# Performance work log

Hardware: AMD Instinct MI355X
Metric: run time of the kernel (lower is better)

## Reference

```python
import jax, jax.numpy as jnp
import numpy as np

EDGE_TYPES = 7
TIME_STEP = 5
STATE_DIM = 1024


def setup_inputs() -> dict:
    key = jax.random.key(0)
    ks = jax.random.split(key, 8)
    B, T, N, DF = 4, 15, 15, 25600
    S, E = STATE_DIM, EDGE_TYPES
    # weights ~ N(0, 0.01), biases zero, matching _initialization()
    return {
        "pose_features": jax.random.normal(ks[0], (B, T, N, DF), jnp.float32),
        "W_compress": jax.random.normal(ks[1], (DF, S), jnp.float32) * 0.01,
        "b_compress": jnp.zeros((S,), jnp.float32),
        "W_edge": jax.random.normal(ks[2], (E, S, S), jnp.float32) * 0.01,
        "b_edge": jnp.zeros((E, S), jnp.float32),
        "W_att": jax.random.normal(ks[3], (E, 2 * S), jnp.float32) * 0.01,
        "b_att": jnp.zeros((E,), jnp.float32),
        "W_r": jax.random.normal(ks[4], (2 * S, S), jnp.float32) * 0.01,
        "b_r": jnp.zeros((S,), jnp.float32),
        "W_z": jax.random.normal(ks[5], (2 * S, S), jnp.float32) * 0.01,
        "b_z": jnp.zeros((S,), jnp.float32),
        "W_h": jax.random.normal(ks[6], (2 * S, S), jnp.float32) * 0.01,
        "b_h": jnp.zeros((S,), jnp.float32),
    }


def reference(pose_features, W_compress, b_compress, W_edge, b_edge,
              W_att, b_att, W_r, b_r, W_z, b_z, W_h, b_h):
    B, T, N, DF = pose_features.shape
    S = W_compress.shape[1]
    E = W_edge.shape[0]
    x = pose_features.reshape(B * T, N, DF)
    prop = x @ W_compress + b_compress                      # [M, N, S]
    # attention Linear over concat(row, col) == row-part + col-part (rank-1 broadcast,
    # avoids materializing the [M, N, N, 2S] repeat/cat tensor; identical math)
    Wa_row, Wa_col = W_att[:, :S], W_att[:, S:]
    scores = None
    for _ in range(1 + TIME_STEP):
        msg = jnp.einsum('bnd,edh->benh', prop, W_edge) + b_edge[None, :, None, :]  # [M,E,N,S]
        row = jnp.einsum('bend,ed->ben', msg, Wa_row)       # [M, E, N]
        col = jnp.einsum('bend,ed->ben', msg, Wa_col)
        scores = jax.nn.sigmoid(row[..., :, None] + col[..., None, :]
                                + b_att[None, :, None, None])   # [M, E, N, N]
        merged = jnp.einsum('beij,bejd->bid', scores, msg)  # [M, N, S]
        a = jnp.concatenate([merged, prop], axis=-1)        # [M, N, 2S]
        r = jax.nn.sigmoid(a @ W_r + b_r)
        z = jax.nn.sigmoid(a @ W_z + b_z)
        h_hat = jnp.tanh(jnp.concatenate([merged, r * prop], axis=-1) @ W_h + b_h)
        prop = (1 - z) * prop + z * h_hat
    box_states = scores.transpose(0, 2, 3, 1)               # [M, N, N, E]
    action_score = ((1 - box_states[..., 0:1]) * box_states).sum(axis=2)
    action_score = action_score.reshape(B, T, N, E)
    actor_score = (1 - box_states[..., 0]).reshape(B, T, N, N)
    acty_score = jax.nn.softmax(
        (action_score * actor_score.sum(axis=-1)[..., None]).sum(axis=2)[:, :, 1:],
        axis=-1)
    return action_score, acty_score, actor_score
```

## Files before the change

kernel.cpp:

```cpp
#include <hip/hip_runtime.h>
#include <hip/hip_bf16.h>

typedef unsigned short bf16_t;
typedef __bf16 bf16x8 __attribute__((ext_vector_type(8)));
typedef float f32x4 __attribute__((ext_vector_type(4)));

__device__ __forceinline__ unsigned short f2bf(float x){
  union { __hip_bfloat16 h; unsigned short u; } c;
  c.h = __float2bfloat16(x);
  return c.u;
}
__device__ __forceinline__ float bf2f(bf16_t u){
  union { unsigned short u; __hip_bfloat16 h; } c;
  c.u = u;
  return __bfloat162float(c.h);
}

#define GL2L(g, l) __builtin_amdgcn_global_load_lds( \
    (const __attribute__((address_space(1))) unsigned int*)(g), \
    (__attribute__((address_space(3))) unsigned int*)(l), 16, 0, 0)

template<int ACT, int MAP>
__global__ __launch_bounds__(256)
void gemm_bf16(const bf16_t* __restrict__ A, int lda,
               const bf16_t* __restrict__ Bt, int ldb,
               float* __restrict__ C, int ldc, size_t csplit,
               const float* __restrict__ bias,
               int M, int N, int K, int Kchunk)
{
  __shared__ __align__(16) bf16_t As[4][128*32];
  __shared__ __align__(16) bf16_t Bs[4][128*32];
  const int tid = threadIdx.x;
  const int w = tid >> 6, lane = tid & 63;
  const int wm = w >> 1, wn = w & 1;
  const int lr = lane & 15, kq = lane >> 4;
  int bcol, brow, bks;
  if (MAP == 0) { bcol = blockIdx.x; brow = blockIdx.y; bks = blockIdx.z; }
  else          { bks = blockIdx.x;  bcol = blockIdx.y; brow = blockIdx.z; }
  const int gm0 = brow * 128, gn0 = bcol * 128;
  const int k0 = bks * Kchunk;
  const int nt = (min(k0 + Kchunk, K) - k0) >> 5;

  const int srow = lane >> 2;
  const int scol = ((lane & 3) ^ ((srow >> 1) & 3)) << 3;
  const int am0 = min(gm0 + w*32 + srow,      M-1);
  const int am1 = min(gm0 + w*32 + 16 + srow, M-1);
  const int bn0 = min(gn0 + w*32 + srow,      N-1);
  const int bn1 = min(gn0 + w*32 + 16 + srow, N-1);
  const bf16_t* Ag0 = A  + (size_t)am0*lda + scol;
  const bf16_t* Ag1 = A  + (size_t)am1*lda + scol;
  const bf16_t* Bg0 = Bt + (size_t)bn0*ldb + scol;
  const bf16_t* Bg1 = Bt + (size_t)bn1*ldb + scol;

  auto STAGEF = [&](int t) {
    const int bsel = t & 3;
    const int kk = k0 + (t << 5);
    char* al = (char*)(&As[bsel][0]) + w*2048;
    char* bl = (char*)(&Bs[bsel][0]) + w*2048;
    GL2L(Ag0 + kk, al);
    GL2L(Ag1 + kk, al + 1024);
    GL2L(Bg0 + kk, bl);
    GL2L(Bg1 + kk, bl + 1024);
  };

  STAGEF(0);
  if (nt > 1) STAGEF(1);
  if (nt > 2) STAGEF(2);

  const int kqs = kq ^ ((lr >> 1) & 3);
  f32x4 acc[4][4] = {};

  for (int t = 0; t < nt; ++t) {
    const int rem = nt - t;
    if (rem >= 3)      { asm volatile("s_waitcnt vmcnt(8)" ::: "memory"); }
    else if (rem == 2) { asm volatile("s_waitcnt vmcnt(4)" ::: "memory"); }
    else               { asm volatile("s_waitcnt vmcnt(0)" ::: "memory"); }
    __builtin_amdgcn_s_barrier();
    __builtin_amdgcn_sched_barrier(0);
    if (t + 3 < nt) STAGEF(t + 3);
    const int bsel = t & 3;
    const char* Ab = (const char*)(&As[bsel][0]);
    const char* Bb = (const char*)(&Bs[bsel][0]);
    bf16x8 af[4], bfr[4];
#pragma unroll
    for (int mi = 0; mi < 4; mi++)
      af[mi] = *(const bf16x8*)(Ab + ((wm*64 + mi*16 + lr) << 6) + (kqs << 4));
#pragma unroll
    for (int ni = 0; ni < 4; ni++)
      bfr[ni] = *(const bf16x8*)(Bb + ((wn*64 + ni*16 + lr) << 6) + (kqs << 4));
    __builtin_amdgcn_s_setprio(1);
#pragma unroll
    for (int mi = 0; mi < 4; mi++)
#pragma unroll
      for (int ni = 0; ni < 4; ni++)
        acc[mi][ni] = __builtin_amdgcn_mfma_f32_16x16x32_bf16(af[mi], bfr[ni], acc[mi][ni], 0, 0, 0);
    __builtin_amdgcn_s_setprio(0);
    __builtin_amdgcn_sched_barrier(0);
  }

#pragma unroll
  for (int mi = 0; mi < 4; mi++) {
#pragma unroll
    for (int ni = 0; ni < 4; ni++) {
      const int col = gn0 + wn*64 + ni*16 + lr;
      const float bv = (ACT == 4) ? bias[col] : 0.f;
#pragma unroll
      for (int i = 0; i < 4; i++) {
        const int row = gm0 + wm*64 + mi*16 + kq*4 + i;
        if (row < M) {
          const float v = acc[mi][ni][i] + bv;
          if (ACT == 4) ((bf16_t*)C)[(size_t)row*ldc + col] = f2bf(v);
          else C[(size_t)bks*csplit + (size_t)row*ldc + col] = v;
        }
      }
    }
  }
}

__global__ void reduce_compress(const float* __restrict__ part, const float* __restrict__ bias,
                                float* __restrict__ prop, bf16_t* __restrict__ xr)
{
  const int idx = blockIdx.x*256 + threadIdx.x;
  const int m = idx >> 10, d = idx & 1023;
  float v = bias[d];
#pragma unroll
  for (int z = 0; z < 8; z++) v += part[(size_t)z*921600 + idx];
  prop[idx] = v;
  xr[(size_t)m*2048 + 1024 + d] = f2bf(v);
}

__global__ void reduce_rz(const float* __restrict__ part, const float* __restrict__ bias,
                          const float* __restrict__ prop, float* __restrict__ Zbuf,
                          bf16_t* __restrict__ Xh)
{
  const int idx = blockIdx.x*256 + threadIdx.x;
  const int m = idx >> 11, c = idx & 2047;
  float v = part[idx] + part[1843200 + idx] + bias[c];
  v = 1.f / (1.f + __expf(-v));
  if (c < 1024) Xh[(size_t)m*2048 + 1024 + c] = f2bf(v * prop[(size_t)m*1024 + c]);
  else          Zbuf[(size_t)m*1024 + (c - 1024)] = v;
}

__global__ void reduce_h(const float* __restrict__ part, const float* __restrict__ bias,
                         const float* __restrict__ Zbuf, float* __restrict__ prop,
                         bf16_t* __restrict__ X)
{
  const int idx = blockIdx.x*256 + threadIdx.x;
  const int m = idx >> 10, d = idx & 1023;
  float v = bias[d];
#pragma unroll
  for (int z = 0; z < 4; z++) v += part[(size_t)z*921600 + idx];
  v = tanhf(v);
  const float zz = Zbuf[idx];
  const float pn = (1.f - zz)*prop[idx] + zz*v;
  prop[idx] = pn;
  X[(size_t)m*2048 + 1024 + d] = f2bf(pn);
}

__global__ void compute_u(const float* __restrict__ We, const float* __restrict__ Wa,
                          float* __restrict__ u_row, float* __restrict__ u_col)
{
  const int w = threadIdx.x >> 6, lane = threadIdx.x & 63;
  const int idx = blockIdx.x*4 + w;
  const int e = idx >> 10, h = idx & 1023;
  const float* wep = We + ((size_t)e*1024 + h)*1024;
  const float* wr  = Wa + (size_t)e*2048;
  const float* wc  = wr + 1024;
  float ar = 0.f, ac = 0.f;
#pragma unroll
  for (int t = 0; t < 16; t++) {
    const float v = wep[lane + 64*t];
    ar += v*wr[lane + 64*t];
    ac += v*wc[lane + 64*t];
  }
  for (int off = 32; off; off >>= 1) { ar += __shfl_down(ar, off); ac += __shfl_down(ac, off); }
  if (lane == 0) { u_row[idx] = ar; u_col[idx] = ac; }
}

__global__ void crc_kernel(const float* __restrict__ be, const float* __restrict__ Wa,
                           float* __restrict__ crc)
{
  const int w = threadIdx.x >> 6, lane = threadIdx.x & 63;
  for (int idx = w; idx < 14; idx += 4) {
    const int e = idx >> 1, which = idx & 1;
    const float* bp = be + e*1024;
    const float* wp = Wa + (size_t)e*2048 + which*1024;
    float a = 0.f;
#pragma unroll
    for (int t = 0; t < 16; t++) a += bp[lane + 64*t]*wp[lane + 64*t];
    for (int off = 32; off; off >>= 1) a += __shfl_down(a, off);
    if (lane == 0) crc[which*7 + e] = a;
  }
}

__global__ void attn_kernel(const float* __restrict__ prop, const float* __restrict__ u_row,
                            const float* __restrict__ u_col, const float* __restrict__ crc,
                            const float* __restrict__ b_att, float* __restrict__ scores)
{
  const int b = blockIdx.x, e = blockIdx.y;
  __shared__ float rowv[15], colv[15];
  const int w = threadIdx.x >> 6, lane = threadIdx.x & 63;
  const float* ur = u_row + (size_t)e*1024;
  const float* uc = u_col + (size_t)e*1024;
  for (int n = w; n < 15; n += 4) {
    const float* pr = prop + (size_t)(b*15 + n)*1024;
    float ar = 0.f, ac = 0.f;
#pragma unroll
    for (int t = 0; t < 16; t++) {
      const float pv = pr[lane + 64*t];
      ar += pv*ur[lane + 64*t];
      ac += pv*uc[lane + 64*t];
    }
    for (int off = 32; off; off >>= 1) { ar += __shfl_down(ar, off); ac += __shfl_down(ac, off); }
    if (lane == 0) { rowv[n] = ar; colv[n] = ac; }
  }
  __syncthreads();
  const float base = b_att[e] + crc[e] + crc[7 + e];
  for (int idx = threadIdx.x; idx < 225; idx += 256) {
    const int i = idx/15, j = idx - i*15;
    const float s = 1.f / (1.f + __expf(-(rowv[i] + colv[j] + base)));
    scores[((size_t)(b*7 + e)*15 + i)*15 + j] = s;
  }
}

__global__ void merged_kernel(const bf16_t* __restrict__ msg, const float* __restrict__ scores,
                              bf16_t* __restrict__ X, bf16_t* __restrict__ Xh)
{
  const int b = blockIdx.x, c = blockIdx.y;
  __shared__ float ms[15*7*128];
  __shared__ float sc[1575];
  for (int q = threadIdx.x; q < 3360; q += 256) {
    const int idx = q*4;
    const int j = idx / 896;
    const int rem = idx - j*896;
    const int e = rem >> 7, dl = rem & 127;
    const ushort4 v = *(const ushort4*)(msg + (size_t)(b*15 + j)*7168 + e*1024 + c*128 + dl);
    ms[idx]   = bf2f(v.x);
    ms[idx+1] = bf2f(v.y);
    ms[idx+2] = bf2f(v.z);
    ms[idx+3] = bf2f(v.w);
  }
  for (int idx = threadIdx.x; idx < 1575; idx += 256)
    sc[idx] = scores[(size_t)b*1575 + idx];
  __syncthreads();
  for (int oi = threadIdx.x; oi < 1920; oi += 256) {
    const int i = oi >> 7, dl = oi & 127;
    float acc = 0.f;
#pragma unroll
    for (int e = 0; e < 7; e++)
#pragma unroll
      for (int j = 0; j < 15; j++)
        acc += sc[(e*15 + i)*15 + j] * ms[j*896 + e*128 + dl];
    const bf16_t o = f2bf(acc);
    X [(size_t)(b*15 + i)*2048 + c*128 + dl] = o;
    Xh[(size_t)(b*15 + i)*2048 + c*128 + dl] = o;
  }
}

__global__ void transpose_k(const float* __restrict__ in, bf16_t* __restrict__ out,
                            int R, int C, int out_ld, size_t in_batch, size_t out_batch)
{
  __shared__ float t[64][65];
  in  += (size_t)blockIdx.z * in_batch;
  out += (size_t)blockIdx.z * out_batch;
  const int r0 = blockIdx.x*64, c0 = blockIdx.y*64;
  const int tc = threadIdx.x & 63, tr = threadIdx.x >> 6;
#pragma unroll
  for (int i = 0; i < 16; i++) {
    const int r = tr*16 + i;
    t[r][tc] = in[(size_t)(r0 + r)*C + c0 + tc];
  }
  __syncthreads();
#pragma unroll
  for (int i = 0; i < 16; i++) {
    const int rr = tr*16 + i;
    out[(size_t)(c0 + rr)*out_ld + r0 + tc] = f2bf(t[tc][rr]);
  }
}

__global__ void cast_f32_bf16(const float4* __restrict__ in, ushort4* __restrict__ out, int n4)
{
  int i = blockIdx.x*256 + threadIdx.x;
  const int stride = gridDim.x*256;
  for (; i < n4; i += stride) {
    const float4 v = in[i];
    out[i] = make_ushort4(f2bf(v.x), f2bf(v.y), f2bf(v.z), f2bf(v.w));
  }
}

__global__ void cat2_kernel(const float* __restrict__ a, const float* __restrict__ b,
                            float* __restrict__ o)
{
  const int i = blockIdx.x*256 + threadIdx.x;
  if (i < 1024) o[i] = a[i];
  else if (i < 2048) o[i] = b[i - 1024];
}

__global__ void finalize_kernel(const float* __restrict__ scores, float* __restrict__ out)
{
  const int b = blockIdx.x;
  __shared__ float sc[1575];
  __shared__ float act[105];
  __shared__ float asum[15];
  __shared__ float t2[7];
  for (int idx = threadIdx.x; idx < 1575; idx += 256)
    sc[idx] = scores[(size_t)b*1575 + idx];
  __syncthreads();
  for (int idx = threadIdx.x; idx < 105; idx += 256) {
    const int i = idx/7, e = idx - i*7;
    float a = 0.f;
#pragma unroll
    for (int j = 0; j < 15; j++)
      a += (1.f - sc[i*15 + j]) * sc[(e*15 + i)*15 + j];
    act[idx] = a;
    out[(size_t)b*105 + idx] = a;
  }
  for (int idx = threadIdx.x; idx < 225; idx += 256) {
    const int i = idx/15, j = idx - i*15;
    out[6660 + (size_t)b*225 + idx] = 1.f - sc[i*15 + j];
  }
  if (threadIdx.x < 15) {
    const int i = threadIdx.x;
    float s = 0.f;
#pragma unroll
    for (int j = 0; j < 15; j++) s += 1.f - sc[i*15 + j];
    asum[i] = s;
  }
  __syncthreads();
  if (threadIdx.x < 7) {
    const int e = threadIdx.x;
    float t = 0.f;
#pragma unroll
    for (int i = 0; i < 15; i++) t += act[i*7 + e]*asum[i];
    t2[e] = t;
  }
  __syncthreads();
  if (threadIdx.x == 0) {
    float mx = -1e30f;
    for (int e = 1; e < 7; e++) mx = fmaxf(mx, t2[e]);
    float s = 0.f, ex[6];
    for (int e = 1; e < 7; e++) { ex[e-1] = __expf(t2[e] - mx); s += ex[e-1]; }
    for (int e = 1; e < 7; e++) out[6300 + (size_t)b*6 + (e-1)] = ex[e-1]/s;
  }
}

extern "C" void kernel_launch(void* const* d_in, const int* in_sizes, int n_in,
                              void* d_out, int out_size, void* d_ws, size_t ws_size,
                              hipStream_t stream)
{
  const float* pose = (const float*)d_in[0];
  const float* Wc   = (const float*)d_in[1];
  const float* bc   = (const float*)d_in[2];
  const float* We   = (const float*)d_in[3];
  const float* be   = (const float*)d_in[4];
  const float* Wa   = (const float*)d_in[5];
  const float* ba   = (const float*)d_in[6];
  const float* Wr   = (const float*)d_in[7];
  const float* br   = (const float*)d_in[8];
  const float* Wz   = (const float*)d_in[9];
  const float* bz   = (const float*)d_in[10];
  const float* Wh   = (const float*)d_in[11];
  const float* bh   = (const float*)d_in[12];
  float* out = (float*)d_out;

  char* p = (char*)d_ws;
  auto alloc = [&](size_t b) { char* r = p; p += (b + 255) & ~(size_t)255; return r; };
  bf16_t* Wedge_t = (bf16_t*)alloc(7168ull*1024*2);
  bf16_t* Wrz_t   = (bf16_t*)alloc(2048ull*2048*2);
  bf16_t* Wh_t    = (bf16_t*)alloc(1024ull*2048*2);
  bf16_t* X       = (bf16_t*)alloc(900ull*2048*2);
  float*  prop    = (float*) alloc(900ull*1024*4);
  float*  scores  = (float*) alloc(60ull*7*15*15*4);
  float*  u_row   = (float*) alloc(7168*4);
  float*  u_col   = (float*) alloc(7168*4);
  float*  crc     = (float*) alloc(64);
  float*  brzv    = (float*) alloc(2048*4);
  char* r1 = alloc(128000000ull);
  bf16_t* Abf     = (bf16_t*)r1;
  bf16_t* Wct     = (bf16_t*)(r1 + 46080000ull);
  float*  partial = (float*) (r1 + 46080000ull + 52428800ull);
  bf16_t* msgb    = (bf16_t*)r1;
  float*  Zbuf    = (float*) (r1 + 12902400ull);
  bf16_t* Xh      = (bf16_t*)(r1 + 16588800ull);
  float*  partRZ  = (float*) (r1 + 20275200ull);
  float*  partH   = (float*) (r1 + 49766400ull);

  compute_u<<<1792, 256, 0, stream>>>(We, Wa, u_row, u_col);
  crc_kernel<<<1, 256, 0, stream>>>(be, Wa, crc);
  cast_f32_bf16<<<2048, 256, 0, stream>>>((const float4*)pose, (ushort4*)Abf, 23040000/4);
  transpose_k<<<dim3(400,16,1), 256, 0, stream>>>(Wc, Wct, 25600, 1024, 25600, 0, 0);
  transpose_k<<<dim3(16,16,7),  256, 0, stream>>>(We, Wedge_t, 1024, 1024, 1024,
                                                  1024ull*1024, 1024ull*1024);
  transpose_k<<<dim3(32,16,1),  256, 0, stream>>>(Wr, Wrz_t, 2048, 1024, 2048, 0, 0);
  transpose_k<<<dim3(32,16,1),  256, 0, stream>>>(Wz, Wrz_t + 1024ull*2048, 2048, 1024, 2048, 0, 0);
  transpose_k<<<dim3(32,16,1),  256, 0, stream>>>(Wh, Wh_t, 2048, 1024, 2048, 0, 0);
  cat2_kernel<<<8, 256, 0, stream>>>(br, bz, brzv);

  gemm_bf16<0,1><<<dim3(8,8,8), 256, 0, stream>>>(Abf, 25600, Wct, 25600,
      partial, 1024, 921600ull, nullptr, 900, 1024, 25600, 3200);
  reduce_compress<<<3600, 256, 0, stream>>>(partial, bc, prop, X);

  for (int it = 0; it < 6; it++) {
    attn_kernel<<<dim3(60,7), 256, 0, stream>>>(prop, u_row, u_col, crc, ba, scores);
    if (it == 5) break;
    gemm_bf16<4,0><<<dim3(56,8,1), 256, 0, stream>>>(X + 1024, 2048, Wedge_t, 1024,
        (float*)msgb, 7168, 0, be, 900, 7168, 1024, 1024);
    merged_kernel<<<dim3(60,8), 256, 0, stream>>>(msgb, scores, X, Xh);
    gemm_bf16<0,0><<<dim3(16,8,2), 256, 0, stream>>>(X, 2048, Wrz_t, 2048,
        partRZ, 2048, 1843200ull, nullptr, 900, 2048, 2048, 1024);
    reduce_rz<<<7200, 256, 0, stream>>>(partRZ, brzv, prop, Zbuf, Xh);
    gemm_bf16<0,0><<<dim3(8,8,4), 256, 0, stream>>>(Xh, 2048, Wh_t, 2048,
        partH, 1024, 921600ull, nullptr, 900, 1024, 2048, 512);
    reduce_h<<<3600, 256, 0, stream>>>(partH, bh, Zbuf, prop, X);
  }

  finalize_kernel<<<60, 256, 0, stream>>>(scores, out);
}
```

Measured before the change: 747.9 us.

## Pack GEMM operands into pre-swizzled 128x32 tile-contiguous bf16 layout

Replaces the row-major bf16 operands and transposed weights with a packed layout in which each 128x32 tile is contiguous and already XOR-swizzled, so each wave's global-to-LDS loads read one contiguous 1 KB span. The separate cast and transpose kernels become pack_a and pack_b, which convert and tile in one pass. The reduce and merged kernels now write activations directly into the packed layout through pidx. This is meant to make the GEMM loads coalesced and drop row-stride address math, at the cost of scattered 2-byte writes in the elementwise kernels.

New measurement: 802.5 us. 1.07x slower.

```diff
diff --git a/kernel.cpp b/kernel.cpp
--- a/kernel.cpp
+++ b/kernel.cpp
@@ -20,13 +20,19 @@
     (const __attribute__((address_space(1))) unsigned int*)(g), \
     (__attribute__((address_space(3))) unsigned int*)(l), 16, 0, 0)
 
+__device__ __forceinline__ size_t pidx(int m, int k, int KT){
+  const int r = m & 127, c = (k >> 3) & 3;
+  const int cs = c ^ ((r >> 1) & 3);
+  return ((size_t)((m >> 7)*KT + (k >> 5)))*4096 + r*32 + cs*8 + (k & 7);
+}
+
 template<int ACT, int MAP>
 __global__ __launch_bounds__(256)
-void gemm_bf16(const bf16_t* __restrict__ A, int lda,
-               const bf16_t* __restrict__ Bt, int ldb,
+void gemm_bf16(const bf16_t* __restrict__ Apk, int KTA, int ka0,
+               const bf16_t* __restrict__ Bpk, int KTB,
                float* __restrict__ C, int ldc, size_t csplit,
                const float* __restrict__ bias,
-               int M, int N, int K, int Kchunk)
+               int M, int KchunkT)
 {
   __shared__ __align__(16) bf16_t As[4][128*32];
   __shared__ __align__(16) bf16_t Bs[4][128*32];
@@ -38,29 +44,20 @@
   if (MAP == 0) { bcol = blockIdx.x; brow = blockIdx.y; bks = blockIdx.z; }
   else          { bks = blockIdx.x;  bcol = blockIdx.y; brow = blockIdx.z; }
   const int gm0 = brow * 128, gn0 = bcol * 128;
-  const int k0 = bks * Kchunk;
-  const int nt = (min(k0 + Kchunk, K) - k0) >> 5;
-
-  const int srow = lane >> 2;
-  const int scol = ((lane & 3) ^ ((srow >> 1) & 3)) << 3;
-  const int am0 = min(gm0 + w*32 + srow,      M-1);
-  const int am1 = min(gm0 + w*32 + 16 + srow, M-1);
-  const int bn0 = min(gn0 + w*32 + srow,      N-1);
-  const int bn1 = min(gn0 + w*32 + 16 + srow, N-1);
-  const bf16_t* Ag0 = A  + (size_t)am0*lda + scol;
-  const bf16_t* Ag1 = A  + (size_t)am1*lda + scol;
-  const bf16_t* Bg0 = Bt + (size_t)bn0*ldb + scol;
-  const bf16_t* Bg1 = Bt + (size_t)bn1*ldb + scol;
+  const int nt = KchunkT;
+  const int kbase = bks * KchunkT;
+
+  const bf16_t* Agt = Apk + ((size_t)brow*KTA + ka0 + kbase)*4096 + (w << 10) + (lane << 3);
+  const bf16_t* Bgt = Bpk + ((size_t)bcol*KTB + kbase)*4096 + (w << 10) + (lane << 3);
 
   auto STAGEF = [&](int t) {
     const int bsel = t & 3;
-    const int kk = k0 + (t << 5);
     char* al = (char*)(&As[bsel][0]) + w*2048;
     char* bl = (char*)(&Bs[bsel][0]) + w*2048;
-    GL2L(Ag0 + kk, al);
-    GL2L(Ag1 + kk, al + 1024);
-    GL2L(Bg0 + kk, bl);
-    GL2L(Bg1 + kk, bl + 1024);
+    const bf16_t* ag = Agt + (size_t)t*4096;
+    const bf16_t* bg = Bgt + (size_t)t*4096;
+    GL2L(ag, al);       GL2L(ag + 512, al + 1024);
+    GL2L(bg, bl);       GL2L(bg + 512, bl + 1024);
   };
 
   STAGEF(0);
@@ -117,8 +114,47 @@
   }
 }
 
+__global__ void pack_a(const float* __restrict__ src, bf16_t* __restrict__ dst,
+                       int M, int srcldK, int KT)
+{
+  const int rt = blockIdx.x, kt = blockIdx.y;
+  bf16_t* dt = dst + ((size_t)rt*KT + kt)*4096;
+  for (int u = threadIdx.x; u < 512; u += 256) {
+    const int r = u >> 2, c = u & 3;
+    const int cs = c ^ ((r >> 1) & 3);
+    const int gm = min(rt*128 + r, M-1);
+    const float4* sp = (const float4*)(src + (size_t)gm*srcldK + kt*32 + c*8);
+    const float4 v0 = sp[0], v1 = sp[1];
+    *(ushort4*)(dt + r*32 + cs*8)     = make_ushort4(f2bf(v0.x), f2bf(v0.y), f2bf(v0.z), f2bf(v0.w));
+    *(ushort4*)(dt + r*32 + cs*8 + 4) = make_ushort4(f2bf(v1.x), f2bf(v1.y), f2bf(v1.z), f2bf(v1.w));
+  }
+}
+
+__global__ void pack_b(const float* __restrict__ src, bf16_t* __restrict__ dst,
+                       int srcldN, int KT, int n0t, size_t in_batch, size_t out_batch)
+{
+  const int ntb = blockIdx.x, kt = blockIdx.y, bz = blockIdx.z;
+  src += (size_t)bz * in_batch;
+  dst += (size_t)bz * out_batch;
+  __shared__ float s[32][132];
+  for (int i = threadIdx.x; i < 4096; i += 256) {
+    const int kl = i >> 7, nl = i & 127;
+    s[kl][nl] = src[(size_t)(kt*32 + kl)*srcldN + ntb*128 + nl];
+  }
+  __syncthreads();
+  bf16_t* dt = dst + ((size_t)(n0t + ntb)*KT + kt)*4096;
+  for (int u = threadIdx.x; u < 512; u += 256) {
+    const int r = u >> 2, c = u & 3;
+    const int cs = c ^ ((r >> 1) & 3);
+    *(ushort4*)(dt + r*32 + cs*8) =
+      make_ushort4(f2bf(s[c*8+0][r]), f2bf(s[c*8+1][r]), f2bf(s[c*8+2][r]), f2bf(s[c*8+3][r]));
+    *(ushort4*)(dt + r*32 + cs*8 + 4) =
+      make_ushort4(f2bf(s[c*8+4][r]), f2bf(s[c*8+5][r]), f2bf(s[c*8+6][r]), f2bf(s[c*8+7][r]));
+  }
+}
+
 __global__ void reduce_compress(const float* __restrict__ part, const float* __restrict__ bias,
-                                float* __restrict__ prop, bf16_t* __restrict__ xr)
+                                float* __restrict__ prop, bf16_t* __restrict__ Xp)
 {
   const int idx = blockIdx.x*256 + threadIdx.x;
   const int m = idx >> 10, d = idx & 1023;
@@ -126,24 +162,24 @@
 #pragma unroll
   for (int z = 0; z < 8; z++) v += part[(size_t)z*921600 + idx];
   prop[idx] = v;
-  xr[(size_t)m*2048 + 1024 + d] = f2bf(v);
+  Xp[pidx(m, 1024 + d, 64)] = f2bf(v);
 }
 
 __global__ void reduce_rz(const float* __restrict__ part, const float* __restrict__ bias,
                           const float* __restrict__ prop, float* __restrict__ Zbuf,
-                          bf16_t* __restrict__ Xh)
+                          bf16_t* __restrict__ Xhp)
 {
   const int idx = blockIdx.x*256 + threadIdx.x;
   const int m = idx >> 11, c = idx & 2047;
   float v = part[idx] + part[1843200 + idx] + bias[c];
   v = 1.f / (1.f + __expf(-v));
-  if (c < 1024) Xh[(size_t)m*2048 + 1024 + c] = f2bf(v * prop[(size_t)m*1024 + c]);
+  if (c < 1024) Xhp[pidx(m, 1024 + c, 64)] = f2bf(v * prop[(size_t)m*1024 + c]);
   else          Zbuf[(size_t)m*1024 + (c - 1024)] = v;
 }
 
 __global__ void reduce_h(const float* __restrict__ part, const float* __restrict__ bias,
                          const float* __restrict__ Zbuf, float* __restrict__ prop,
-                         bf16_t* __restrict__ X)
+                         bf16_t* __restrict__ Xp)
 {
   const int idx = blockIdx.x*256 + threadIdx.x;
   const int m = idx >> 10, d = idx & 1023;
@@ -154,7 +190,7 @@
   const float zz = Zbuf[idx];
   const float pn = (1.f - zz)*prop[idx] + zz*v;
   prop[idx] = pn;
-  X[(size_t)m*2048 + 1024 + d] = f2bf(pn);
+  Xp[pidx(m, 1024 + d, 64)] = f2bf(pn);
 }
 
 __global__ void compute_u(const float* __restrict__ We, const float* __restrict__ Wa,
@@ -224,7 +260,7 @@
 }
 
 __global__ void merged_kernel(const bf16_t* __restrict__ msg, const float* __restrict__ scores,
-                              bf16_t* __restrict__ X, bf16_t* __restrict__ Xh)
+                              bf16_t* __restrict__ Xp, bf16_t* __restrict__ Xhp)
 {
   const int b = blockIdx.x, c = blockIdx.y;
   __shared__ float ms[15*7*128];
@@ -252,39 +288,9 @@
       for (int j = 0; j < 15; j++)
         acc += sc[(e*15 + i)*15 + j] * ms[j*896 + e*128 + dl];
     const bf16_t o = f2bf(acc);
-    X [(size_t)(b*15 + i)*2048 + c*128 + dl] = o;
-    Xh[(size_t)(b*15 + i)*2048 + c*128 + dl] = o;
-  }
-}
-
-__global__ void transpose_k(const float* __restrict__ in, bf16_t* __restrict__ out,
-                            int R, int C, int out_ld, size_t in_batch, size_t out_batch)
-{
-  __shared__ float t[64][65];
-  in  += (size_t)blockIdx.z * in_batch;
-  out += (size_t)blockIdx.z * out_batch;
-  const int r0 = blockIdx.x*64, c0 = blockIdx.y*64;
-  const int tc = threadIdx.x & 63, tr = threadIdx.x >> 6;
-#pragma unroll
-  for (int i = 0; i < 16; i++) {
-    const int r = tr*16 + i;
-    t[r][tc] = in[(size_t)(r0 + r)*C + c0 + tc];
-  }
-  __syncthreads();
-#pragma unroll
-  for (int i = 0; i < 16; i++) {
-    const int rr = tr*16 + i;
-    out[(size_t)(c0 + rr)*out_ld + r0 + tc] = f2bf(t[tc][rr]);
-  }
-}
-
-__global__ void cast_f32_bf16(const float4* __restrict__ in, ushort4* __restrict__ out, int n4)
-{
-  int i = blockIdx.x*256 + threadIdx.x;
-  const int stride = gridDim.x*256;
-  for (; i < n4; i += stride) {
-    const float4 v = in[i];
-    out[i] = make_ushort4(f2bf(v.x), f2bf(v.y), f2bf(v.z), f2bf(v.w));
+    const int m = b*15 + i, k = c*128 + dl;
+    Xp [pidx(m, k, 64)] = o;
+    Xhp[pidx(m, k, 64)] = o;
   }
 }
 
@@ -365,53 +371,53 @@
 
   char* p = (char*)d_ws;
   auto alloc = [&](size_t b) { char* r = p; p += (b + 255) & ~(size_t)255; return r; };
-  bf16_t* Wedge_t = (bf16_t*)alloc(7168ull*1024*2);
-  bf16_t* Wrz_t   = (bf16_t*)alloc(2048ull*2048*2);
-  bf16_t* Wh_t    = (bf16_t*)alloc(1024ull*2048*2);
-  bf16_t* X       = (bf16_t*)alloc(900ull*2048*2);
-  float*  prop    = (float*) alloc(900ull*1024*4);
-  float*  scores  = (float*) alloc(60ull*7*15*15*4);
-  float*  u_row   = (float*) alloc(7168*4);
-  float*  u_col   = (float*) alloc(7168*4);
-  float*  crc     = (float*) alloc(64);
-  float*  brzv    = (float*) alloc(2048*4);
-  char* r1 = alloc(128000000ull);
-  bf16_t* Abf     = (bf16_t*)r1;
-  bf16_t* Wct     = (bf16_t*)(r1 + 46080000ull);
-  float*  partial = (float*) (r1 + 46080000ull + 52428800ull);
+  bf16_t* Wedgep = (bf16_t*)alloc(56ull*32*8192);
+  bf16_t* Wrzp   = (bf16_t*)alloc(16ull*64*8192);
+  bf16_t* Whp    = (bf16_t*)alloc(8ull*64*8192);
+  bf16_t* Xp     = (bf16_t*)alloc(8ull*64*8192);
+  bf16_t* Xhp    = (bf16_t*)alloc(8ull*64*8192);
+  float*  prop   = (float*) alloc(900ull*1024*4);
+  float*  scores = (float*) alloc(60ull*7*15*15*4);
+  float*  u_row  = (float*) alloc(7168*4);
+  float*  u_col  = (float*) alloc(7168*4);
+  float*  crc    = (float*) alloc(64);
+  float*  brzv   = (float*) alloc(2048*4);
+  char* r1 = alloc(134400000ull);
+  bf16_t* Apk     = (bf16_t*)r1;
+  bf16_t* Wcp     = (bf16_t*)(r1 + 52428800ull);
+  float*  partial = (float*) (r1 + 2ull*52428800ull);
   bf16_t* msgb    = (bf16_t*)r1;
   float*  Zbuf    = (float*) (r1 + 12902400ull);
-  bf16_t* Xh      = (bf16_t*)(r1 + 16588800ull);
-  float*  partRZ  = (float*) (r1 + 20275200ull);
-  float*  partH   = (float*) (r1 + 49766400ull);
+  float*  partRZ  = (float*) (r1 + 12902400ull + 3686400ull);
+  float*  partH   = (float*) (r1 + 12902400ull + 3686400ull + 14745600ull);
 
   compute_u<<<1792, 256, 0, stream>>>(We, Wa, u_row, u_col);
   crc_kernel<<<1, 256, 0, stream>>>(be, Wa, crc);
-  cast_f32_bf16<<<2048, 256, 0, stream>>>((const float4*)pose, (ushort4*)Abf, 23040000/4);
-  transpose_k<<<dim3(400,16,1), 256, 0, stream>>>(Wc, Wct, 25600, 1024, 25600, 0, 0);
-  transpose_k<<<dim3(16,16,7),  256, 0, stream>>>(We, Wedge_t, 1024, 1024, 1024,
-                                                  1024ull*1024, 1024ull*1024);
-  transpose_k<<<dim3(32,16,1),  256, 0, stream>>>(Wr, Wrz_t, 2048, 1024, 2048, 0, 0);
-  transpose_k<<<dim3(32,16,1),  256, 0, stream>>>(Wz, Wrz_t + 1024ull*2048, 2048, 1024, 2048, 0, 0);
-  transpose_k<<<dim3(32,16,1),  256, 0, stream>>>(Wh, Wh_t, 2048, 1024, 2048, 0, 0);
   cat2_kernel<<<8, 256, 0, stream>>>(br, bz, brzv);
-
-  gemm_bf16<0,1><<<dim3(8,8,8), 256, 0, stream>>>(Abf, 25600, Wct, 25600,
-      partial, 1024, 921600ull, nullptr, 900, 1024, 25600, 3200);
-  reduce_compress<<<3600, 256, 0, stream>>>(partial, bc, prop, X);
+  pack_a<<<dim3(8,800), 256, 0, stream>>>(pose, Apk, 900, 25600, 800);
+  pack_b<<<dim3(8,800), 256, 0, stream>>>(Wc, Wcp, 1024, 800, 0, 0, 0);
+  pack_b<<<dim3(8,32,7), 256, 0, stream>>>(We, Wedgep, 1024, 32, 0,
+                                           1024ull*1024, 8ull*32*4096);
+  pack_b<<<dim3(8,64), 256, 0, stream>>>(Wr, Wrzp, 1024, 64, 0, 0, 0);
+  pack_b<<<dim3(8,64), 256, 0, stream>>>(Wz, Wrzp, 1024, 64, 8, 0, 0);
+  pack_b<<<dim3(8,64), 256, 0, stream>>>(Wh, Whp, 1024, 64, 0, 0, 0);
+
+  gemm_bf16<0,1><<<dim3(8,8,8), 256, 0, stream>>>(Apk, 800, 0, Wcp, 800,
+      partial, 1024, 921600ull, nullptr, 900, 100);
+  reduce_compress<<<3600, 256, 0, stream>>>(partial, bc, prop, Xp);
 
   for (int it = 0; it < 6; it++) {
     attn_kernel<<<dim3(60,7), 256, 0, stream>>>(prop, u_row, u_col, crc, ba, scores);
     if (it == 5) break;
-    gemm_bf16<4,0><<<dim3(56,8,1), 256, 0, stream>>>(X + 1024, 2048, Wedge_t, 1024,
-        (float*)msgb, 7168, 0, be, 900, 7168, 1024, 1024);
-    merged_kernel<<<dim3(60,8), 256, 0, stream>>>(msgb, scores, X, Xh);
-    gemm_bf16<0,0><<<dim3(16,8,2), 256, 0, stream>>>(X, 2048, Wrz_t, 2048,
-        partRZ, 2048, 1843200ull, nullptr, 900, 2048, 2048, 1024);
-    reduce_rz<<<7200, 256, 0, stream>>>(partRZ, brzv, prop, Zbuf, Xh);
-    gemm_bf16<0,0><<<dim3(8,8,4), 256, 0, stream>>>(Xh, 2048, Wh_t, 2048,
-        partH, 1024, 921600ull, nullptr, 900, 1024, 2048, 512);
-    reduce_h<<<3600, 256, 0, stream>>>(partH, bh, Zbuf, prop, X);
+    gemm_bf16<4,0><<<dim3(56,8,1), 256, 0, stream>>>(Xp, 64, 32, Wedgep, 32,
+        (float*)msgb, 7168, 0, be, 900, 32);
+    merged_kernel<<<dim3(60,8), 256, 0, stream>>>(msgb, scores, Xp, Xhp);
+    gemm_bf16<0,0><<<dim3(16,8,2), 256, 0, stream>>>(Xp, 64, 0, Wrzp, 64,
+        partRZ, 2048, 1843200ull, nullptr, 900, 32);
+    reduce_rz<<<7200, 256, 0, stream>>>(partRZ, brzv, prop, Zbuf, Xhp);
+    gemm_bf16<0,0><<<dim3(8,8,4), 256, 0, stream>>>(Xhp, 64, 0, Whp, 64,
+        partH, 1024, 921600ull, nullptr, 900, 16);
+    reduce_h<<<3600, 256, 0, stream>>>(partH, bh, Zbuf, prop, Xp);
   }
 
   finalize_kernel<<<60, 256, 0, stream>>>(scores, out);
```
